# Kernel tuning notes

Hardware: AMD Instinct MI355X
Metric: run time of the kernel (lower is better)

Reference implementation:

```python
import jax, jax.numpy as jnp
import numpy as np

N_NODES = 100000
N_EDGES = 1600000
IN_FEATS = 64
HIDDEN = 64
NUM_CLASSES = 2


def setup_inputs() -> dict:
    key = jax.random.key(0)
    ks = jax.random.split(key, 9)
    feat = jax.random.normal(ks[0], (N_NODES, IN_FEATS), dtype=jnp.float32)
    src = jax.random.randint(ks[1], (N_EDGES,), 0, N_NODES, dtype=jnp.int64) if jax.config.jax_enable_x64 else jax.random.randint(ks[1], (N_EDGES,), 0, N_NODES).astype(jnp.int32)
    dst = jax.random.randint(ks[2], (N_EDGES,), 0, N_NODES).astype(src.dtype)
    s_in = 1.0 / np.sqrt(IN_FEATS)
    s_e = 1.0 / np.sqrt(2 * HIDDEN)
    s_o = 1.0 / np.sqrt(HIDDEN)
    W_in = jax.random.uniform(ks[3], (IN_FEATS, HIDDEN), jnp.float32, -s_in, s_in)
    b_in = jax.random.uniform(ks[4], (HIDDEN,), jnp.float32, -s_in, s_in)
    W_edge = jax.random.uniform(ks[5], (2 * HIDDEN, 1), jnp.float32, -s_e, s_e)
    b_edge = jax.random.uniform(ks[6], (1,), jnp.float32, -s_e, s_e)
    W_out = jax.random.uniform(ks[7], (HIDDEN, NUM_CLASSES), jnp.float32, -s_o, s_o)
    b_out = jax.random.uniform(ks[8], (NUM_CLASSES,), jnp.float32, -s_o, s_o)
    return {"feat": feat, "src": src, "dst": dst, "W_in": W_in, "b_in": b_in,
            "W_edge": W_edge, "b_edge": b_edge, "W_out": W_out, "b_out": b_out}


def reference(feat, src, dst, W_in, b_in, W_edge, b_edge, W_out, b_out):
    # input node MLP: [N, in] @ [in, H]
    h = feat @ W_in + b_in  # [N, H]
    # edge function: sigmoid(Linear(cat(h_src, h_dst))) -- split concat to avoid [E, 2H] buffer
    hu = h[src]  # [E, H]
    hv = h[dst]  # [E, H]
    W_u, W_v = W_edge[:HIDDEN], W_edge[HIDDEN:]  # each [H, 1]
    w = jax.nn.sigmoid(hu @ W_u + hv @ W_v + b_edge)  # [E, 1]
    # message = h_src * w, reduce = sum over incoming edges at dst
    msgs = hu * w  # [E, H]
    agg = jax.ops.segment_sum(msgs, dst, num_segments=N_NODES)  # [N, H]
    # DGL UDF-reduce semantics: zero in-degree nodes keep previous h
    deg = jax.ops.segment_sum(jnp.ones((dst.shape[0],), dtype=jnp.float32), dst, num_segments=N_NODES)
    h_new = jnp.where(deg[:, None] > 0, agg, h)
    return h_new @ W_out + b_out  # [N, num_classes]
```

## Files before the change

### kernel.cpp

```cpp
#include <hip/hip_runtime.h>
#include <math.h>

#define N_NODES 100000
#define N_EDGES 1600000

#define BK_LOG 8
#define BKW 256
#define NBK ((N_NODES + BKW - 1) / BKW)
#define CAPB 4864
#define UNS4 3

#define GS 800
#define EPS (N_EDGES / GS)
#define EPS4 (EPS / 4)

#define NT_BLOCKS ((N_NODES + 63) / 64)

__global__ __launch_bounds__(256) void prep_kernel(
    const float* __restrict__ feat,
    const float* __restrict__ W_in,
    const float* __restrict__ b_in,
    const float* __restrict__ W_edge,
    const float* __restrict__ W_out,
    const int*   __restrict__ src,
    const int*   __restrict__ dst,
    int* __restrict__ cursor,
    int* __restrict__ ework,
    float4* __restrict__ nodeT)
{
    const int tid = threadIdx.x;

    if ((int)blockIdx.x >= NT_BLOCKS) {
        __shared__ int hist[NBK];
        __shared__ int base[NBK];
        for (int i = tid; i < NBK; i += 256) hist[i] = 0;
        __syncthreads();

        const int4* src4 = (const int4*)src;
        const int4* dst4 = (const int4*)dst;
        const int   b40  = ((blockIdx.x - NT_BLOCKS) * EPS) >> 2;

        int bb[8], rr[8], pk[8];
        #pragma unroll
        for (int j = 0; j < 2; ++j) {
            const int o4 = j * 256 + tid;
            if (o4 < EPS4) {
                const int4 d4 = dst4[b40 + o4];
                const int4 s4 = src4[b40 + o4];
                const int dv[4] = {d4.x, d4.y, d4.z, d4.w};
                const int sv[4] = {s4.x, s4.y, s4.z, s4.w};
                #pragma unroll
                for (int u = 0; u < 4; ++u) {
                    const int idx = j * 4 + u;
                    const int d = dv[u];
                    const int b = d >> BK_LOG;
                    bb[idx] = b;
                    rr[idx] = atomicAdd(&hist[b], 1);
                    pk[idx] = ((d & (BKW - 1)) << 17) | sv[u];
                }
            }
        }
        __syncthreads();

        for (int b = tid; b < NBK; b += 256) {
            const int c = hist[b];
            if (c) base[b] = atomicAdd(&cursor[b], c);
        }
        __syncthreads();

        #pragma unroll
        for (int j = 0; j < 2; ++j) {
            const int o4 = j * 256 + tid;
            if (o4 < EPS4) {
                #pragma unroll
                for (int u = 0; u < 4; ++u) {
                    const int idx = j * 4 + u;
                    ework[bb[idx] * CAPB + base[bb[idx]] + rr[idx]] = pk[idx];
                }
            }
        }
        return;
    }

    __shared__ float sP[64 * 4];
    __shared__ float sQ[64 * 4];
    __shared__ float sc[4];

    if (tid < 64) {
        sP[tid * 4 + 0] = W_edge[tid];
        sP[tid * 4 + 1] = W_out[tid * 2 + 0];
        sP[tid * 4 + 2] = W_out[tid * 2 + 1];
        sP[tid * 4 + 3] = W_edge[64 + tid];
    }
    __syncthreads();

    {
        const int k = tid >> 2, j = tid & 3;
        float q = 0.f;
        for (int m = 0; m < 64; ++m) q += W_in[k * 64 + m] * sP[m * 4 + j];
        sQ[k * 4 + j] = q;
        if (tid < 4) {
            float cc = 0.f;
            for (int m = 0; m < 64; ++m) cc += b_in[m] * sP[m * 4 + tid];
            sc[tid] = cc;
        }
    }
    __syncthreads();

    const int lane = tid & 63;
    const int wv   = tid >> 6;
    const int n    = blockIdx.x * 64 + wv * 16 + (lane >> 2);
    const int ks   = (lane & 3) << 4;

    float p0 = 0.f, p1 = 0.f, p2 = 0.f, p3 = 0.f;
    if (n < N_NODES) {
        const float* fr = feat + (size_t)n * 64 + ks;
        #pragma unroll
        for (int i4 = 0; i4 < 4; ++i4) {
            const float4 f = *(const float4*)(fr + i4 * 4);
            const float fv[4] = {f.x, f.y, f.z, f.w};
            #pragma unroll
            for (int u = 0; u < 4; ++u) {
                const float4 q = *(const float4*)&sQ[(ks + i4 * 4 + u) * 4];
                p0 += fv[u] * q.x;
                p1 += fv[u] * q.y;
                p2 += fv[u] * q.z;
                p3 += fv[u] * q.w;
            }
        }
    }
    #pragma unroll
    for (int off = 1; off <= 2; off <<= 1) {
        p0 += __shfl_xor(p0, off);
        p1 += __shfl_xor(p1, off);
        p2 += __shfl_xor(p2, off);
        p3 += __shfl_xor(p3, off);
    }
    if (n < N_NODES && (lane & 3) == 0)
        nodeT[n] = make_float4(p0 + sc[0], p1 + sc[1], p2 + sc[2], p3 + sc[3]);
}

__global__ __launch_bounds__(512) void sortagg_kernel(
    const int* __restrict__ ework,
    const int* __restrict__ cursor,
    const float4* __restrict__ nodeT,
    const float* __restrict__ b_edge,
    const float* __restrict__ b_out,
    float2* __restrict__ out)
{
    __shared__ int hist[BKW];
    __shared__ int sdata[BKW];
    __shared__ int sbase[BKW];
    __shared__ int ssorted[CAPB];

    const int b   = blockIdx.x;
    const int tid = threadIdx.x;

    if (tid < BKW) hist[tid] = 0;
    __syncthreads();

    const int cnt = min(cursor[b], CAPB);
    const int4* ew4 = (const int4*)(ework + b * CAPB);

    int4 vv[UNS4];
    int  rk[UNS4][4];
    #pragma unroll
    for (int j = 0; j < UNS4; ++j) {
        const int o = (j * 512 + tid) * 4;
        if (o < cnt) {
            const int4 v = ew4[j * 512 + tid];
            vv[j] = v;
            const int ve[4] = {v.x, v.y, v.z, v.w};
            #pragma unroll
            for (int u = 0; u < 4; ++u)
                if (o + u < cnt) rk[j][u] = atomicAdd(&hist[ve[u] >> 17], 1);
        }
    }
    __syncthreads();

    int own = 0;
    if (tid < BKW) { own = hist[tid]; sdata[tid] = own; }
    __syncthreads();
    for (int off = 1; off < BKW; off <<= 1) {
        int t = 0;
        if (tid < BKW && tid >= off) t = sdata[tid - off];
        __syncthreads();
        if (tid < BKW) sdata[tid] += t;
        __syncthreads();
    }
    if (tid < BKW) sbase[tid] = sdata[tid] - own;
    __syncthreads();

    #pragma unroll
    for (int j = 0; j < UNS4; ++j) {
        const int o = (j * 512 + tid) * 4;
        if (o < cnt) {
            const int4 v = vv[j];
            const int ve[4] = {v.x, v.y, v.z, v.w};
            #pragma unroll
            for (int u = 0; u < 4; ++u)
                if (o + u < cnt)
                    ssorted[sbase[ve[u] >> 17] + rk[j][u]] = ve[u] & 0x1FFFF;
        }
    }
    __syncthreads();

    const int sub = tid & 3;
    const float be  = b_edge[0];
    const float bo0 = b_out[0];
    const float bo1 = b_out[1];

    #pragma unroll
    for (int pass = 0; pass < 2; ++pass) {
        const int l = pass * 128 + (tid >> 2);
        const int n = b * BKW + l;

        float4 tn = make_float4(0.f, 0.f, 0.f, 0.f);
        if (n < N_NODES) tn = nodeT[n];
        const int   beg = sbase[l];
        const int   len = hist[l];
        const float Bn  = tn.w + be;

        float m0 = 0.f, m1 = 0.f;
        for (int i = sub; i < len; i += 4) {
            const int    s = ssorted[beg + i];
            const float4 t = nodeT[s];
            const float  w = 1.0f / (1.0f + __expf(-(t.x + Bn)));
            m0 += w * t.y;
            m1 += w * t.z;
        }
        m0 += __shfl_xor(m0, 1);
        m1 += __shfl_xor(m1, 1);
        m0 += __shfl_xor(m0, 2);
        m1 += __shfl_xor(m1, 2);

        if (sub == 0 && n < N_NODES) {
            const float o0 = (len ? m0 : tn.y) + bo0;
            const float o1 = (len ? m1 : tn.z) + bo1;
            out[n] = make_float2(o0, o1);
        }
    }
}

extern "C" void kernel_launch(void* const* d_in, const int* in_sizes, int n_in,
                              void* d_out, int out_size, void* d_ws, size_t ws_size,
                              hipStream_t stream) {
    const float* feat   = (const float*)d_in[0];
    const int*   src    = (const int*)d_in[1];
    const int*   dst    = (const int*)d_in[2];
    const float* W_in   = (const float*)d_in[3];
    const float* b_in   = (const float*)d_in[4];
    const float* W_edge = (const float*)d_in[5];
    const float* b_edge = (const float*)d_in[6];
    const float* W_out  = (const float*)d_in[7];
    const float* b_out  = (const float*)d_in[8];
    float2* out = (float2*)d_out;

    float4* nodeT  = (float4*)d_ws;
    int*    ework  = (int*)(nodeT + N_NODES);
    int*    cursor = ework + NBK * CAPB;

    hipMemsetAsync(cursor, 0, NBK * sizeof(int), stream);

    prep_kernel<<<NT_BLOCKS + GS, 256, 0, stream>>>(
        feat, W_in, b_in, W_edge, W_out, src, dst, cursor, ework, nodeT);
    sortagg_kernel<<<NBK, 512, 0, stream>>>(
        ework, cursor, nodeT, b_edge, b_out, out);
}
```

Before: 132.7 us.

## Halve bucket width, reorder prep blocks, wave-shuffle scan, unroll gather loop

Buckets shrink from 256 to 128 destination nodes, so sortagg runs twice as many 256-thread blocks with less shared memory each, which should help occupancy and load balance. The edge-bucketing blocks now come before the node-transform blocks in prep, and each handles twice as many edges. The shared-memory Hillis-Steele scan becomes a wavefront shuffle scan with a cross-wave total, cutting barriers. The gather loop is unrolled by two to overlap the random nodeT loads, at the cost of tighter bucket capacity (2688 slots for about 2048 expected edges) and more registers.

```diff
diff --git a/kernel.cpp b/kernel.cpp
--- a/kernel.cpp
+++ b/kernel.cpp
@@ -4,13 +4,13 @@
 #define N_NODES 100000
 #define N_EDGES 1600000
 
-#define BK_LOG 8
-#define BKW 256
+#define BK_LOG 7
+#define BKW 128
 #define NBK ((N_NODES + BKW - 1) / BKW)
-#define CAPB 4864
+#define CAPB 2688
 #define UNS4 3
 
-#define GS 800
+#define GS 400
 #define EPS (N_EDGES / GS)
 #define EPS4 (EPS / 4)
 
@@ -30,7 +30,7 @@
 {
     const int tid = threadIdx.x;
 
-    if ((int)blockIdx.x >= NT_BLOCKS) {
+    if ((int)blockIdx.x < GS) {
         __shared__ int hist[NBK];
         __shared__ int base[NBK];
         for (int i = tid; i < NBK; i += 256) hist[i] = 0;
@@ -38,11 +38,11 @@
 
         const int4* src4 = (const int4*)src;
         const int4* dst4 = (const int4*)dst;
-        const int   b40  = ((blockIdx.x - NT_BLOCKS) * EPS) >> 2;
-
-        int bb[8], rr[8], pk[8];
+        const int   b40  = (int)blockIdx.x * EPS4;
+
+        int bb[16], rr[16], pk[16];
         #pragma unroll
-        for (int j = 0; j < 2; ++j) {
+        for (int j = 0; j < 4; ++j) {
             const int o4 = j * 256 + tid;
             if (o4 < EPS4) {
                 const int4 d4 = dst4[b40 + o4];
@@ -69,7 +69,7 @@
         __syncthreads();
 
         #pragma unroll
-        for (int j = 0; j < 2; ++j) {
+        for (int j = 0; j < 4; ++j) {
             const int o4 = j * 256 + tid;
             if (o4 < EPS4) {
                 #pragma unroll
@@ -109,7 +109,7 @@
 
     const int lane = tid & 63;
     const int wv   = tid >> 6;
-    const int n    = blockIdx.x * 64 + wv * 16 + (lane >> 2);
+    const int n    = ((int)blockIdx.x - GS) * 64 + wv * 16 + (lane >> 2);
     const int ks   = (lane & 3) << 4;
 
     float p0 = 0.f, p1 = 0.f, p2 = 0.f, p3 = 0.f;
@@ -140,7 +140,7 @@
         nodeT[n] = make_float4(p0 + sc[0], p1 + sc[1], p2 + sc[2], p3 + sc[3]);
 }
 
-__global__ __launch_bounds__(512) void sortagg_kernel(
+__global__ __launch_bounds__(256) void sortagg_kernel(
     const int* __restrict__ ework,
     const int* __restrict__ cursor,
     const float4* __restrict__ nodeT,
@@ -149,8 +149,8 @@
     float2* __restrict__ out)
 {
     __shared__ int hist[BKW];
-    __shared__ int sdata[BKW];
     __shared__ int sbase[BKW];
+    __shared__ int wtot[2];
     __shared__ int ssorted[CAPB];
 
     const int b   = blockIdx.x;
@@ -166,9 +166,9 @@
     int  rk[UNS4][4];
     #pragma unroll
     for (int j = 0; j < UNS4; ++j) {
-        const int o = (j * 512 + tid) * 4;
+        const int o = (j * 256 + tid) * 4;
         if (o < cnt) {
-            const int4 v = ew4[j * 512 + tid];
+            const int4 v = ew4[j * 256 + tid];
             vv[j] = v;
             const int ve[4] = {v.x, v.y, v.z, v.w};
             #pragma unroll
@@ -178,22 +178,21 @@
     }
     __syncthreads();
 
-    int own = 0;
-    if (tid < BKW) { own = hist[tid]; sdata[tid] = own; }
-    __syncthreads();
-    for (int off = 1; off < BKW; off <<= 1) {
-        int t = 0;
-        if (tid < BKW && tid >= off) t = sdata[tid - off];
-        __syncthreads();
-        if (tid < BKW) sdata[tid] += t;
-        __syncthreads();
-    }
-    if (tid < BKW) sbase[tid] = sdata[tid] - own;
+    int own = 0, inc = 0;
+    if (tid < BKW) { own = hist[tid]; inc = own; }
+    #pragma unroll
+    for (int off = 1; off < 64; off <<= 1) {
+        const int t = __shfl_up(inc, off);
+        if ((tid & 63) >= off) inc += t;
+    }
+    if (tid < BKW && (tid & 63) == 63) wtot[tid >> 6] = inc;
+    __syncthreads();
+    if (tid < BKW) sbase[tid] = inc - own + ((tid >= 64) ? wtot[0] : 0);
     __syncthreads();
 
     #pragma unroll
     for (int j = 0; j < UNS4; ++j) {
-        const int o = (j * 512 + tid) * 4;
+        const int o = (j * 256 + tid) * 4;
         if (o < cnt) {
             const int4 v = vv[j];
             const int ve[4] = {v.x, v.y, v.z, v.w};
@@ -212,7 +211,7 @@
 
     #pragma unroll
     for (int pass = 0; pass < 2; ++pass) {
-        const int l = pass * 128 + (tid >> 2);
+        const int l = pass * 64 + (tid >> 2);
         const int n = b * BKW + l;
 
         float4 tn = make_float4(0.f, 0.f, 0.f, 0.f);
@@ -222,12 +221,23 @@
         const float Bn  = tn.w + be;
 
         float m0 = 0.f, m1 = 0.f;
-        for (int i = sub; i < len; i += 4) {
-            const int    s = ssorted[beg + i];
-            const float4 t = nodeT[s];
-            const float  w = 1.0f / (1.0f + __expf(-(t.x + Bn)));
-            m0 += w * t.y;
-            m1 += w * t.z;
+        int i = sub;
+        for (; i + 4 < len; i += 8) {
+            const int s0 = ssorted[beg + i];
+            const int s1 = ssorted[beg + i + 4];
+            const float4 t0 = nodeT[s0];
+            const float4 t1 = nodeT[s1];
+            const float w0 = 1.0f / (1.0f + __expf(-(t0.x + Bn)));
+            const float w1 = 1.0f / (1.0f + __expf(-(t1.x + Bn)));
+            m0 += w0 * t0.y + w1 * t1.y;
+            m1 += w0 * t0.z + w1 * t1.z;
+        }
+        if (i < len) {
+            const int s0 = ssorted[beg + i];
+            const float4 t0 = nodeT[s0];
+            const float w0 = 1.0f / (1.0f + __expf(-(t0.x + Bn)));
+            m0 += w0 * t0.y;
+            m1 += w0 * t0.z;
         }
         m0 += __shfl_xor(m0, 1);
         m1 += __shfl_xor(m1, 1);
@@ -262,8 +272,8 @@
 
     hipMemsetAsync(cursor, 0, NBK * sizeof(int), stream);
 
-    prep_kernel<<<NT_BLOCKS + GS, 256, 0, stream>>>(
+    prep_kernel<<<GS + NT_BLOCKS, 256, 0, stream>>>(
         feat, W_in, b_in, W_edge, W_out, src, dst, cursor, ework, nodeT);
-    sortagg_kernel<<<NBK, 512, 0, stream>>>(
+    sortagg_kernel<<<NBK, 256, 0, stream>>>(
         ework, cursor, nodeT, b_edge, b_out, out);
 }
```

New measurement: 127.1 us. 1.04x faster.

## Replace bucket-sort aggregation with direct float atomic scatter per edge

Applied to the files above, without the earlier changes.

Drops the two-level bucket sort of edges by destination and the per-bucket segmented reduction. Each edge now computes its sigmoid weight and scatters the two projected message components and an in-degree count into a per-node accumulator with unsafe float atomics, and a small final kernel applies the zero-degree fallback and the output bias. This removes the ework staging buffer, the shared-memory histograms and scans, and the per-bucket capacity limit. In exchange it issues three global atomics per edge at random addresses, summation order becomes nondeterministic, and there is one more kernel launch.

```diff
diff --git a/kernel.cpp b/kernel.cpp
--- a/kernel.cpp
+++ b/kernel.cpp
@@ -4,83 +4,22 @@
 #define N_NODES 100000
 #define N_EDGES 1600000
 
-#define BK_LOG 8
-#define BKW 256
-#define NBK ((N_NODES + BKW - 1) / BKW)
-#define CAPB 4864
-#define UNS4 3
+#define NT_BLOCKS ((N_NODES + 63) / 64)
+#define E4 (N_EDGES / 4)
+#define E_BLOCKS ((E4 + 255) / 256)
 
-#define GS 800
-#define EPS (N_EDGES / GS)
-#define EPS4 (EPS / 4)
+typedef int i32x4 __attribute__((ext_vector_type(4)));
 
-#define NT_BLOCKS ((N_NODES + 63) / 64)
-
-__global__ __launch_bounds__(256) void prep_kernel(
+__global__ __launch_bounds__(256) void node_kernel(
     const float* __restrict__ feat,
     const float* __restrict__ W_in,
     const float* __restrict__ b_in,
     const float* __restrict__ W_edge,
     const float* __restrict__ W_out,
-    const int*   __restrict__ src,
-    const int*   __restrict__ dst,
-    int* __restrict__ cursor,
-    int* __restrict__ ework,
-    float4* __restrict__ nodeT)
+    float4* __restrict__ nodeT,
+    float4* __restrict__ agg)
 {
     const int tid = threadIdx.x;
-
-    if ((int)blockIdx.x >= NT_BLOCKS) {
-        __shared__ int hist[NBK];
-        __shared__ int base[NBK];
-        for (int i = tid; i < NBK; i += 256) hist[i] = 0;
-        __syncthreads();
-
-        const int4* src4 = (const int4*)src;
-        const int4* dst4 = (const int4*)dst;
-        const int   b40  = ((blockIdx.x - NT_BLOCKS) * EPS) >> 2;
-
-        int bb[8], rr[8], pk[8];
-        #pragma unroll
-        for (int j = 0; j < 2; ++j) {
-            const int o4 = j * 256 + tid;
-            if (o4 < EPS4) {
-                const int4 d4 = dst4[b40 + o4];
-                const int4 s4 = src4[b40 + o4];
-                const int dv[4] = {d4.x, d4.y, d4.z, d4.w};
-                const int sv[4] = {s4.x, s4.y, s4.z, s4.w};
-                #pragma unroll
-                for (int u = 0; u < 4; ++u) {
-                    const int idx = j * 4 + u;
-                    const int d = dv[u];
-                    const int b = d >> BK_LOG;
-                    bb[idx] = b;
-                    rr[idx] = atomicAdd(&hist[b], 1);
-                    pk[idx] = ((d & (BKW - 1)) << 17) | sv[u];
-                }
-            }
-        }
-        __syncthreads();
-
-        for (int b = tid; b < NBK; b += 256) {
-            const int c = hist[b];
-            if (c) base[b] = atomicAdd(&cursor[b], c);
-        }
-        __syncthreads();
-
-        #pragma unroll
-        for (int j = 0; j < 2; ++j) {
-            const int o4 = j * 256 + tid;
-            if (o4 < EPS4) {
-                #pragma unroll
-                for (int u = 0; u < 4; ++u) {
-                    const int idx = j * 4 + u;
-                    ework[bb[idx] * CAPB + base[bb[idx]] + rr[idx]] = pk[idx];
-                }
-            }
-        }
-        return;
-    }
 
     __shared__ float sP[64 * 4];
     __shared__ float sQ[64 * 4];
@@ -91,6 +30,10 @@
         sP[tid * 4 + 1] = W_out[tid * 2 + 0];
         sP[tid * 4 + 2] = W_out[tid * 2 + 1];
         sP[tid * 4 + 3] = W_edge[64 + tid];
+    }
+    if (tid < 64) {
+        const int n = blockIdx.x * 64 + tid;
+        if (n < N_NODES) agg[n] = make_float4(0.f, 0.f, 0.f, 0.f);
     }
     __syncthreads();
 
@@ -140,106 +83,50 @@
         nodeT[n] = make_float4(p0 + sc[0], p1 + sc[1], p2 + sc[2], p3 + sc[3]);
 }
 
-__global__ __launch_bounds__(512) void sortagg_kernel(
-    const int* __restrict__ ework,
-    const int* __restrict__ cursor,
+__global__ __launch_bounds__(256) void edge_kernel(
+    const int* __restrict__ src,
+    const int* __restrict__ dst,
     const float4* __restrict__ nodeT,
     const float* __restrict__ b_edge,
+    float4* __restrict__ agg)
+{
+    const int idx = blockIdx.x * 256 + threadIdx.x;
+    if (idx >= E4) return;
+
+    const float be = b_edge[0];
+    const i32x4 sv = __builtin_nontemporal_load(((const i32x4*)src) + idx);
+    const i32x4 dv = __builtin_nontemporal_load(((const i32x4*)dst) + idx);
+    const float* nT = (const float*)nodeT;
+
+    #pragma unroll
+    for (int u = 0; u < 4; ++u) {
+        const int s = sv[u];
+        const int d = dv[u];
+        const float4 ts  = nodeT[s];
+        const float  tdw = nT[4 * d + 3];
+        const float  w   = 1.0f / (1.0f + __expf(-(ts.x + tdw + be)));
+        float* a = (float*)&agg[d];
+        unsafeAtomicAdd(a + 0, w * ts.y);
+        unsafeAtomicAdd(a + 1, w * ts.z);
+        unsafeAtomicAdd(a + 2, 1.0f);
+    }
+}
+
+__global__ __launch_bounds__(256) void final_kernel(
+    const float4* __restrict__ nodeT,
+    const float4* __restrict__ agg,
     const float* __restrict__ b_out,
     float2* __restrict__ out)
 {
-    __shared__ int hist[BKW];
-    __shared__ int sdata[BKW];
-    __shared__ int sbase[BKW];
-    __shared__ int ssorted[CAPB];
-
-    const int b   = blockIdx.x;
-    const int tid = threadIdx.x;
-
-    if (tid < BKW) hist[tid] = 0;
-    __syncthreads();
-
-    const int cnt = min(cursor[b], CAPB);
-    const int4* ew4 = (const int4*)(ework + b * CAPB);
-
-    int4 vv[UNS4];
-    int  rk[UNS4][4];
-    #pragma unroll
-    for (int j = 0; j < UNS4; ++j) {
-        const int o = (j * 512 + tid) * 4;
-        if (o < cnt) {
-            const int4 v = ew4[j * 512 + tid];
-            vv[j] = v;
-            const int ve[4] = {v.x, v.y, v.z, v.w};
-            #pragma unroll
-            for (int u = 0; u < 4; ++u)
-                if (o + u < cnt) rk[j][u] = atomicAdd(&hist[ve[u] >> 17], 1);
-        }
-    }
-    __syncthreads();
-
-    int own = 0;
-    if (tid < BKW) { own = hist[tid]; sdata[tid] = own; }
-    __syncthreads();
-    for (int off = 1; off < BKW; off <<= 1) {
-        int t = 0;
-        if (tid < BKW && tid >= off) t = sdata[tid - off];
-        __syncthreads();
-        if (tid < BKW) sdata[tid] += t;
-        __syncthreads();
-    }
-    if (tid < BKW) sbase[tid] = sdata[tid] - own;
-    __syncthreads();
-
-    #pragma unroll
-    for (int j = 0; j < UNS4; ++j) {
-        const int o = (j * 512 + tid) * 4;
-        if (o < cnt) {
-            const int4 v = vv[j];
-            const int ve[4] = {v.x, v.y, v.z, v.w};
-            #pragma unroll
-            for (int u = 0; u < 4; ++u)
-                if (o + u < cnt)
-                    ssorted[sbase[ve[u] >> 17] + rk[j][u]] = ve[u] & 0x1FFFF;
-        }
-    }
-    __syncthreads();
-
-    const int sub = tid & 3;
-    const float be  = b_edge[0];
+    const int n = blockIdx.x * 256 + threadIdx.x;
+    if (n >= N_NODES) return;
+    const float4 a = agg[n];
+    const float4 t = nodeT[n];
     const float bo0 = b_out[0];
     const float bo1 = b_out[1];
-
-    #pragma unroll
-    for (int pass = 0; pass < 2; ++pass) {
-        const int l = pass * 128 + (tid >> 2);
-        const int n = b * BKW + l;
-
-        float4 tn = make_float4(0.f, 0.f, 0.f, 0.f);
-        if (n < N_NODES) tn = nodeT[n];
-        const int   beg = sbase[l];
-        const int   len = hist[l];
-        const float Bn  = tn.w + be;
-
-        float m0 = 0.f, m1 = 0.f;
-        for (int i = sub; i < len; i += 4) {
-            const int    s = ssorted[beg + i];
-            const float4 t = nodeT[s];
-            const float  w = 1.0f / (1.0f + __expf(-(t.x + Bn)));
-            m0 += w * t.y;
-            m1 += w * t.z;
-        }
-        m0 += __shfl_xor(m0, 1);
-        m1 += __shfl_xor(m1, 1);
-        m0 += __shfl_xor(m0, 2);
-        m1 += __shfl_xor(m1, 2);
-
-        if (sub == 0 && n < N_NODES) {
-            const float o0 = (len ? m0 : tn.y) + bo0;
-            const float o1 = (len ? m1 : tn.z) + bo1;
-            out[n] = make_float2(o0, o1);
-        }
-    }
+    const bool  has = a.z > 0.f;
+    out[n] = make_float2((has ? a.x : t.y) + bo0,
+                         (has ? a.y : t.z) + bo1);
 }
 
 extern "C" void kernel_launch(void* const* d_in, const int* in_sizes, int n_in,
@@ -256,14 +143,13 @@
     const float* b_out  = (const float*)d_in[8];
     float2* out = (float2*)d_out;
 
-    float4* nodeT  = (float4*)d_ws;
-    int*    ework  = (int*)(nodeT + N_NODES);
-    int*    cursor = ework + NBK * CAPB;
+    float4* nodeT = (float4*)d_ws;
+    float4* agg   = nodeT + N_NODES;
 
-    hipMemsetAsync(cursor, 0, NBK * sizeof(int), stream);
-
-    prep_kernel<<<NT_BLOCKS + GS, 256, 0, stream>>>(
-        feat, W_in, b_in, W_edge, W_out, src, dst, cursor, ework, nodeT);
-    sortagg_kernel<<<NBK, 512, 0, stream>>>(
-        ework, cursor, nodeT, b_edge, b_out, out);
+    node_kernel<<<NT_BLOCKS, 256, 0, stream>>>(
+        feat, W_in, b_in, W_edge, W_out, nodeT, agg);
+    edge_kernel<<<E_BLOCKS, 256, 0, stream>>>(
+        src, dst, nodeT, b_edge, agg);
+    final_kernel<<<(N_NODES + 255) / 256, 256, 0, stream>>>(
+        nodeT, agg, b_out, out);
 }
```

Result: slower. 342.5 us (+158.0%).
